# Optimization experiments

Hardware: AMD Instinct MI355X
Metric: run time of the kernel (lower is better)

The kernel has to match this reference:

```python
import jax, jax.numpy as jnp
from jax import lax
import numpy as np

D_MODEL = 1024
N_HEADS = 16
D_STATE = D_MODEL // N_HEADS  # 64
EPS = 1e-6


def setup_inputs() -> dict:
    key = jax.random.key(0)
    ks = jax.random.split(key, 8)
    B, S = 4, 4096
    s = 1.0 / np.sqrt(D_MODEL)
    return {
        "x": jax.random.normal(ks[0], (B, S, D_MODEL), dtype=jnp.float32),
        "state": jnp.zeros((B, N_HEADS, D_STATE), dtype=jnp.float32),
        "norm_w": jnp.ones((D_MODEL,), dtype=jnp.float32),
        "Wp": jax.random.normal(ks[1], (D_MODEL, 3 * N_HEADS * D_STATE), dtype=jnp.float32) * s,
        "bp": jax.random.normal(ks[2], (3 * N_HEADS * D_STATE,), dtype=jnp.float32) * 0.01,
        "Wg": jax.random.normal(ks[3], (D_MODEL, D_MODEL), dtype=jnp.float32) * s,
        "bg": jax.random.normal(ks[4], (D_MODEL,), dtype=jnp.float32) * 0.01,
        "Wo": jax.random.normal(ks[5], (D_MODEL, D_MODEL), dtype=jnp.float32) * s,
        "bo": jax.random.normal(ks[6], (D_MODEL,), dtype=jnp.float32) * 0.01,
    }


def reference(x, state, norm_w, Wp, bp, Wg, bg, Wo, bo):
    B, S, D = x.shape
    # RMSNorm
    rms = jnp.sqrt(jnp.mean(x * x, axis=-1, keepdims=True) + EPS)
    xn = norm_w * x / rms
    # input-dependent gate and SSM parameters (all per-timestep, vectorized)
    gate = jax.nn.sigmoid(xn @ Wg + bg)                        # (B,S,D)
    p = (xn @ Wp + bp).reshape(B, S, N_HEADS, 3, D_STATE)
    delta = jax.nn.sigmoid(p[..., 0, :])                       # (B,S,H,Ds)
    Bt = p[..., 1, :]
    Ct = p[..., 2, :]
    # sequential recurrence h_{t+1} = delta_t * h_t + B_t via lax.scan over time
    def step(h, db):
        d, b = db
        h = d * h + b
        return h, h
    dT = jnp.moveaxis(delta, 1, 0)  # (S,B,H,Ds)
    bT = jnp.moveaxis(Bt, 1, 0)
    new_state, hs = lax.scan(step, state, (dT, bT))
    hs = jnp.moveaxis(hs, 0, 1)     # (B,S,H,Ds)
    ssm = (Ct * hs).reshape(B, S, D)
    mixed = gate * ssm + (1.0 - gate) * xn
    y = mixed @ Wo + bo + x         # out_proj + residual (dropout=0)
    return y, new_state
```

## Files before the change

### kernel.cpp

```cpp
#include <hip/hip_runtime.h>
#include <hip/hip_bf16.h>
#include <cstdint>
#include <cstddef>

#define D_MODEL 1024
#define N_HEADS 16
#define D_STATE 64
#define SEQ 4096
#define BATCH 4
#define M_TOK (BATCH * SEQ)
#define N1 4096
#define CLEN 128
#define NCH (SEQ / CLEN)
#define NCHAN (BATCH * D_MODEL)

typedef __attribute__((ext_vector_type(8))) short bf16x8;
typedef __attribute__((ext_vector_type(4))) float f32x4;

__device__ __forceinline__ float sigmoidf_(float x) {
    return 1.0f / (1.0f + __expf(-x));
}

__device__ __forceinline__ void async_load16(const void* g, void* l) {
    __builtin_amdgcn_global_load_lds(
        (__attribute__((address_space(1))) void*)(g),
        (__attribute__((address_space(3))) void*)(l), 16, 0, 0);
}

__global__ __launch_bounds__(256) void transpose_cvt(
    const float* __restrict__ src, __hip_bfloat16* __restrict__ dst,
    int K, int N)
{
    __shared__ float tile[32][33];
    int n0 = blockIdx.x * 32, k0 = blockIdx.y * 32;
    int tx = threadIdx.x, ty = threadIdx.y;
#pragma unroll
    for (int j = 0; j < 32; j += 8)
        tile[ty + j][tx] = src[(size_t)(k0 + ty + j) * N + n0 + tx];
    __syncthreads();
#pragma unroll
    for (int j = 0; j < 32; j += 8)
        dst[(size_t)(n0 + ty + j) * K + k0 + tx] = __float2bfloat16(tile[tx][ty + j]);
}

__global__ __launch_bounds__(256) void rmsnorm_kernel(
    const float* __restrict__ x, const float* __restrict__ w,
    __hip_bfloat16* __restrict__ xn)
{
    int m = blockIdx.x;
    int tid = threadIdx.x;
    const float4* xr = (const float4*)(x + (size_t)m * D_MODEL);
    float4 v = xr[tid];
    float ss = v.x * v.x + v.y * v.y + v.z * v.z + v.w * v.w;
#pragma unroll
    for (int o = 32; o >= 1; o >>= 1) ss += __shfl_xor(ss, o, 64);
    __shared__ float red[4];
    int wave = tid >> 6, lane = tid & 63;
    if (lane == 0) red[wave] = ss;
    __syncthreads();
    float tot = red[0] + red[1] + red[2] + red[3];
    float scale = rsqrtf(tot * (1.0f / D_MODEL) + 1e-6f);
    const float4* wr = (const float4*)w;
    float4 wv = wr[tid];
    __hip_bfloat16 o4[4];
    o4[0] = __float2bfloat16(wv.x * v.x * scale);
    o4[1] = __float2bfloat16(wv.y * v.y * scale);
    o4[2] = __float2bfloat16(wv.z * v.z * scale);
    o4[3] = __float2bfloat16(wv.w * v.w * scale);
    *(uint64_t*)(xn + (size_t)m * D_MODEL + tid * 4) = *(uint64_t*)o4;
}


template <int MODE>
__global__ __launch_bounds__(512, 2) void gemm256(
    const __hip_bfloat16* __restrict__ A,
    const __hip_bfloat16* __restrict__ Bt,
    const float* __restrict__ bias0,
    const float* __restrict__ bias1,
    void* __restrict__ outp, int N, int K)
{
    extern __shared__ short lds[];
    const int tid = threadIdx.x;
    const int wave = tid >> 6, lane = tid & 63;
    const int fr = lane & 15, fq = lane >> 4;
    const int frx = fr & 7;
    const int wm = (wave >> 2) * 128;
    const int wn = (wave & 3) * 64;

    const int gx = gridDim.x;
    const int nwg = gx * gridDim.y;
    const int orig = blockIdx.y * gx + blockIdx.x;
    const int swz = (orig & 7) * (nwg >> 3) + (orig >> 3);
    const int m0 = (swz / gx) * 256;
    const int n0 = (swz % gx) * 256;

    const int rb = tid >> 3, p8 = tid & 7;
    const int lsl = p8 ^ (rb & 7);
    const short* Ag0 = (const short*)A + (size_t)(m0 + rb) * K + lsl * 8;
    const short* Bg0 = (const short*)Bt + (size_t)(n0 + rb) * K + lsl * 8;
    const int stL = rb * 64 + p8 * 8;

    const int NT = K >> 6;

    f32x4 acc[2][4][4];
#pragma unroll
    for (int h = 0; h < 2; ++h)
#pragma unroll
        for (int i = 0; i < 4; ++i)
#pragma unroll
            for (int j = 0; j < 4; ++j)
                acc[h][i][j] = (f32x4){0.f, 0.f, 0.f, 0.f};

    {
        short* la = lds;
        short* lb = lds + 16384;
        async_load16(Bg0 + (size_t)(0 * 64) * K, lb + stL + 0 * 4096);
        async_load16(Bg0 + (size_t)(1 * 64) * K, lb + stL + 1 * 4096);
        async_load16(Bg0 + (size_t)(2 * 64) * K, lb + stL + 2 * 4096);
        async_load16(Bg0 + (size_t)(3 * 64) * K, lb + stL + 3 * 4096);
        async_load16(Ag0 + (size_t)(0 * 64) * K, la + stL + 0 * 4096);
        async_load16(Ag0 + (size_t)(2 * 64) * K, la + stL + 2 * 4096);
        async_load16(Ag0 + (size_t)(1 * 64) * K, la + stL + 1 * 4096);
        async_load16(Ag0 + (size_t)(3 * 64) * K, la + stL + 3 * 4096);
    }
    asm volatile("s_waitcnt vmcnt(2)" ::: "memory");
    __builtin_amdgcn_s_barrier();
    __builtin_amdgcn_sched_barrier(0);

#define LDA(h, i, kk) (*(const bf16x8*)&Ab[(wm + (h)*64 + (i)*16 + fr) * 64 + \
                                           (((kk)*4 + fq) ^ frx) * 8])
#define LDB(j, kk)    (*(const bf16x8*)&Bb[(wn + (j)*16 + fr) * 64 + \
                                           (((kk)*4 + fq) ^ frx) * 8])
#define STAGE_A(c) async_load16(AgN + (size_t)((c) * 64) * K, laN + stL + (c) * 4096)
#define STAGE_B(c) async_load16(BgN + (size_t)((c) * 64) * K, lbN + stL + (c) * 4096)

    for (int t = 0; t < NT; ++t) {
        const short* Ab = lds + ((t & 1) ? 32768 : 0);
        const short* Bb = Ab + 16384;
        short* laN = lds + ((t & 1) ? 0 : 32768);
        short* lbN = laN + 16384;
        const short* AgN = Ag0 + (size_t)(t + 1) * 64;
        const short* BgN = Bg0 + (size_t)(t + 1) * 64;
        const bool pf = (t + 1 < NT);

        bf16x8 af[4][2], b0[2][2], b1[2][2];

#pragma unroll
        for (int i = 0; i < 4; ++i) { af[i][0] = LDA(0, i, 0); af[i][1] = LDA(0, i, 1); }
#pragma unroll
        for (int j = 0; j < 2; ++j) { b0[j][0] = LDB(j, 0); b0[j][1] = LDB(j, 1); }
        if (pf) { STAGE_B(0); STAGE_B(1); }
        __builtin_amdgcn_s_barrier();
        __builtin_amdgcn_sched_barrier(0);
        __builtin_amdgcn_s_setprio(1);
#pragma unroll
        for (int i = 0; i < 4; ++i)
#pragma unroll
            for (int j = 0; j < 2; ++j) {
                acc[0][i][j] = __builtin_amdgcn_mfma_f32_16x16x32_bf16(af[i][0], b0[j][0], acc[0][i][j], 0, 0, 0);
                acc[0][i][j] = __builtin_amdgcn_mfma_f32_16x16x32_bf16(af[i][1], b0[j][1], acc[0][i][j], 0, 0, 0);
            }
        __builtin_amdgcn_s_setprio(0);
        __builtin_amdgcn_sched_barrier(0);
        __builtin_amdgcn_s_barrier();
        __builtin_amdgcn_sched_barrier(0);

#pragma unroll
        for (int j = 0; j < 2; ++j) { b1[j][0] = LDB(2 + j, 0); b1[j][1] = LDB(2 + j, 1); }
        if (pf) { STAGE_B(2); STAGE_B(3); }
        __builtin_amdgcn_s_barrier();
        __builtin_amdgcn_sched_barrier(0);
        __builtin_amdgcn_s_setprio(1);
#pragma unroll
        for (int i = 0; i < 4; ++i)
#pragma unroll
            for (int j = 0; j < 2; ++j) {
                acc[0][i][2 + j] = __builtin_amdgcn_mfma_f32_16x16x32_bf16(af[i][0], b1[j][0], acc[0][i][2 + j], 0, 0, 0);
                acc[0][i][2 + j] = __builtin_amdgcn_mfma_f32_16x16x32_bf16(af[i][1], b1[j][1], acc[0][i][2 + j], 0, 0, 0);
            }
        __builtin_amdgcn_s_setprio(0);
        __builtin_amdgcn_sched_barrier(0);
        if (pf) { asm volatile("s_waitcnt vmcnt(4)" ::: "memory"); }
        else    { asm volatile("s_waitcnt vmcnt(0)" ::: "memory"); }
        __builtin_amdgcn_s_barrier();
        __builtin_amdgcn_sched_barrier(0);

#pragma unroll
        for (int i = 0; i < 4; ++i) { af[i][0] = LDA(1, i, 0); af[i][1] = LDA(1, i, 1); }
        if (pf) { STAGE_A(0); STAGE_A(2); }
        __builtin_amdgcn_s_barrier();
        __builtin_amdgcn_sched_barrier(0);
        __builtin_amdgcn_s_setprio(1);
#pragma unroll
        for (int i = 0; i < 4; ++i)
#pragma unroll
            for (int j = 0; j < 2; ++j) {
                acc[1][i][j] = __builtin_amdgcn_mfma_f32_16x16x32_bf16(af[i][0], b0[j][0], acc[1][i][j], 0, 0, 0);
                acc[1][i][j] = __builtin_amdgcn_mfma_f32_16x16x32_bf16(af[i][1], b0[j][1], acc[1][i][j], 0, 0, 0);
            }
        __builtin_amdgcn_s_setprio(0);
        __builtin_amdgcn_sched_barrier(0);
        __builtin_amdgcn_s_barrier();
        __builtin_amdgcn_sched_barrier(0);

        if (pf) {
            STAGE_A(1); STAGE_A(3);
            asm volatile("s_waitcnt vmcnt(2)" ::: "memory");
        }
        __builtin_amdgcn_s_barrier();
        __builtin_amdgcn_sched_barrier(0);
        __builtin_amdgcn_s_setprio(1);
#pragma unroll
        for (int i = 0; i < 4; ++i)
#pragma unroll
            for (int j = 0; j < 2; ++j) {
                acc[1][i][2 + j] = __builtin_amdgcn_mfma_f32_16x16x32_bf16(af[i][0], b1[j][0], acc[1][i][2 + j], 0, 0, 0);
                acc[1][i][2 + j] = __builtin_amdgcn_mfma_f32_16x16x32_bf16(af[i][1], b1[j][1], acc[1][i][2 + j], 0, 0, 0);
            }
        __builtin_amdgcn_s_setprio(0);
        __builtin_amdgcn_sched_barrier(0);
        __builtin_amdgcn_s_barrier();
        __builtin_amdgcn_sched_barrier(0);
    }
#undef LDA
#undef LDB
#undef STAGE_A
#undef STAGE_B

    if constexpr (MODE == 0) {
        __hip_bfloat16* O = (__hip_bfloat16*)outp;
        float bv[4];
#pragma unroll
        for (int j = 0; j < 4; ++j) {
            int gcol = n0 + wn + j * 16 + fr;
            bv[j] = (gcol < D_MODEL) ? bias0[gcol] : bias1[gcol - D_MODEL];
        }
#pragma unroll
        for (int h = 0; h < 2; ++h)
#pragma unroll
            for (int i = 0; i < 4; ++i)
#pragma unroll
                for (int r = 0; r < 4; ++r) {
                    int grow = m0 + wm + h * 64 + i * 16 + fq * 4 + r;
                    __hip_bfloat16* orow = O + (size_t)grow * N + n0 + wn + fr;
#pragma unroll
                    for (int j = 0; j < 4; ++j)
                        orow[j * 16] = __float2bfloat16(acc[h][i][j][r] + bv[j]);
                }
    } else {
        float* O = (float*)outp;
#pragma unroll
        for (int h = 0; h < 2; ++h)
#pragma unroll
            for (int i = 0; i < 4; ++i)
#pragma unroll
                for (int r = 0; r < 4; ++r) {
                    int grow = m0 + wm + h * 64 + i * 16 + fq * 4 + r;
#pragma unroll
                    for (int j = 0; j < 4; ++j) {
                        int gcol = n0 + wn + j * 16 + fr;
                        O[(size_t)grow * N + gcol] =
                            acc[h][i][j][r] + bias0[gcol] + bias1[(size_t)grow * D_MODEL + gcol];
                    }
                }
    }
}

__global__ __launch_bounds__(256) void scan_part1(
    const __hip_bfloat16* __restrict__ out1,
    float* __restrict__ Abuf, float* __restrict__ Bbuf)
{
    int g = blockIdx.x * 256 + threadIdx.x;
    int chan = g & (NCHAN - 1);
    int c = g >> 12;
    int b = chan >> 10;
    int hd = chan & 1023;
    int h = hd >> 6, d = hd & 63;
    size_t tok0 = (size_t)b * SEQ + (size_t)c * CLEN;
    const __hip_bfloat16* pd = out1 + tok0 * N1 + D_MODEL + h * 192 + d;
    float a = 1.0f, hloc = 0.0f;
#pragma unroll 4
    for (int s = 0; s < CLEN; s++) {
        float dp = __bfloat162float(pd[0]);
        float bt = __bfloat162float(pd[64]);
        float sd = sigmoidf_(dp);
        a *= sd;
        hloc = sd * hloc + bt;
        pd += N1;
    }
    Abuf[c * NCHAN + chan] = a;
    Bbuf[c * NCHAN + chan] = hloc;
}

__global__ __launch_bounds__(256) void scan_comb(
    const float* __restrict__ Abuf, const float* __restrict__ Bbuf,
    const float* __restrict__ state, float* __restrict__ Pbuf,
    float* __restrict__ new_state)
{
    int chan = blockIdx.x * 256 + threadIdx.x;
    float hp = state[chan];
#pragma unroll
    for (int c = 0; c < NCH; c++) {
        Pbuf[c * NCHAN + chan] = hp;
        hp = Abuf[c * NCHAN + chan] * hp + Bbuf[c * NCHAN + chan];
    }
    new_state[chan] = hp;
}

__global__ __launch_bounds__(256) void scan_apply(
    const __hip_bfloat16* __restrict__ out1,
    const __hip_bfloat16* __restrict__ xn,
    const float* __restrict__ Pbuf,
    __hip_bfloat16* __restrict__ mixed)
{
    int g = blockIdx.x * 256 + threadIdx.x;
    int chan = g & (NCHAN - 1);
    int c = g >> 12;
    int b = chan >> 10;
    int hd = chan & 1023;
    int h = hd >> 6, d = hd & 63;
    size_t tok0 = (size_t)b * SEQ + (size_t)c * CLEN;
    const __hip_bfloat16* rbase = out1 + tok0 * N1;
    const __hip_bfloat16* xbase = xn + tok0 * D_MODEL + hd;
    __hip_bfloat16* mbase = mixed + tok0 * D_MODEL + hd;
    const int pcol = D_MODEL + h * 192 + d;
    float hh = Pbuf[c * NCHAN + chan];
#pragma unroll 4
    for (int s = 0; s < CLEN; s++) {
        const __hip_bfloat16* r = rbase + (size_t)s * N1;
        float dp = __bfloat162float(r[pcol]);
        float bt = __bfloat162float(r[pcol + 64]);
        float ct = __bfloat162float(r[pcol + 128]);
        float gp = __bfloat162float(r[hd]);
        float sd = sigmoidf_(dp);
        hh = sd * hh + bt;
        float gg = sigmoidf_(gp);
        float xv = __bfloat162float(xbase[(size_t)s * D_MODEL]);
        mbase[(size_t)s * D_MODEL] = __float2bfloat16(gg * (ct * hh) + (1.0f - gg) * xv);
    }
}

extern "C" void kernel_launch(void* const* d_in, const int* in_sizes, int n_in,
                              void* d_out, int out_size, void* d_ws, size_t ws_size,
                              hipStream_t stream) {
    const float* x      = (const float*)d_in[0];
    const float* state  = (const float*)d_in[1];
    const float* norm_w = (const float*)d_in[2];
    const float* Wp     = (const float*)d_in[3];
    const float* bp     = (const float*)d_in[4];
    const float* Wg     = (const float*)d_in[5];
    const float* bg     = (const float*)d_in[6];
    const float* Wo     = (const float*)d_in[7];
    const float* bo     = (const float*)d_in[8];
    float* out = (float*)d_out;

    __hip_bfloat16* W1T   = (__hip_bfloat16*)d_ws;
    __hip_bfloat16* WoT   = W1T + (size_t)N1 * D_MODEL;
    __hip_bfloat16* xnb   = WoT + (size_t)D_MODEL * D_MODEL;
    __hip_bfloat16* out1  = xnb + (size_t)M_TOK * D_MODEL;
    __hip_bfloat16* mixed = out1 + (size_t)M_TOK * N1;
    float* Abuf = (float*)(mixed + (size_t)M_TOK * D_MODEL);
    float* Bbuf = Abuf + (size_t)NCHAN * NCH;
    float* Pbuf = Bbuf + (size_t)NCHAN * NCH;

    static bool attr_set = false;
    if (!attr_set) {
        hipFuncSetAttribute(reinterpret_cast<const void*>(&gemm256<0>),
                            hipFuncAttributeMaxDynamicSharedMemorySize, 131072);
        hipFuncSetAttribute(reinterpret_cast<const void*>(&gemm256<1>),
                            hipFuncAttributeMaxDynamicSharedMemorySize, 131072);
        attr_set = true;
    }

    dim3 tb(32, 8);
    transpose_cvt<<<dim3(1024 / 32, 1024 / 32), tb, 0, stream>>>(Wg, W1T, 1024, 1024);
    transpose_cvt<<<dim3(3072 / 32, 1024 / 32), tb, 0, stream>>>(
        Wp, W1T + (size_t)D_MODEL * D_MODEL, 1024, 3072);
    transpose_cvt<<<dim3(1024 / 32, 1024 / 32), tb, 0, stream>>>(Wo, WoT, 1024, 1024);

    rmsnorm_kernel<<<M_TOK, 256, 0, stream>>>(x, norm_w, xnb);

    gemm256<0><<<dim3(N1 / 256, M_TOK / 256), 512, 131072, stream>>>(
        xnb, W1T, bg, bp, (void*)out1, N1, D_MODEL);

    scan_part1<<<(NCHAN * NCH) / 256, 256, 0, stream>>>(out1, Abuf, Bbuf);
    scan_comb<<<NCHAN / 256, 256, 0, stream>>>(
        Abuf, Bbuf, state, Pbuf, out + (size_t)M_TOK * D_MODEL);
    scan_apply<<<(NCHAN * NCH) / 256, 256, 0, stream>>>(out1, xnb, Pbuf, mixed);

    gemm256<1><<<dim3(D_MODEL / 256, M_TOK / 256), 512, 131072, stream>>>(
        mixed, WoT, bo, x, (void*)out, D_MODEL, D_MODEL);
}
```

Baseline: 394.1 us.

## Software-pipeline LDS fragment reads across iterations and cut per-iteration barriers

Restructures the GEMM main loop so that the A/B register fragments for the next k-tile are preloaded at the end of the current iteration. LDS reads are interleaved between MFMA blocks instead of sitting in their own barrier-separated phases. Most of the workgroup barriers per iteration are removed, leaving one after the B wait and one after the final A wait. This aims to hide LDS latency and sync overhead, at the cost of more live fragment registers (afA/afB). It also risks a race on reuse of the staged buffers, since fewer barriers protect them.

Result: no change. 391.4 us (-0.7%).

```diff
diff --git a/kernel.cpp b/kernel.cpp
--- a/kernel.cpp
+++ b/kernel.cpp
@@ -127,12 +127,23 @@
     __builtin_amdgcn_s_barrier();
     __builtin_amdgcn_sched_barrier(0);
 
-#define LDA(h, i, kk) (*(const bf16x8*)&Ab[(wm + (h)*64 + (i)*16 + fr) * 64 + \
-                                           (((kk)*4 + fq) ^ frx) * 8])
-#define LDB(j, kk)    (*(const bf16x8*)&Bb[(wn + (j)*16 + fr) * 64 + \
-                                           (((kk)*4 + fq) ^ frx) * 8])
+#define LDA_(base, h, i, kk) (*(const bf16x8*)&(base)[(wm + (h)*64 + (i)*16 + fr) * 64 + \
+                                                      (((kk)*4 + fq) ^ frx) * 8])
+#define LDB_(base, j, kk)    (*(const bf16x8*)&(base)[(wn + (j)*16 + fr) * 64 + \
+                                                      (((kk)*4 + fq) ^ frx) * 8])
 #define STAGE_A(c) async_load16(AgN + (size_t)((c) * 64) * K, laN + stL + (c) * 4096)
 #define STAGE_B(c) async_load16(BgN + (size_t)((c) * 64) * K, lbN + stL + (c) * 4096)
+
+    bf16x8 afA[4][2], afB[4][2], b0[2][2], b1[2][2];
+
+    {
+        const short* Ab = lds;
+        const short* Bb = lds + 16384;
+#pragma unroll
+        for (int i = 0; i < 4; ++i) { afA[i][0] = LDA_(Ab, 0, i, 0); afA[i][1] = LDA_(Ab, 0, i, 1); }
+#pragma unroll
+        for (int j = 0; j < 2; ++j) { b0[j][0] = LDB_(Bb, j, 0); b0[j][1] = LDB_(Bb, j, 1); }
+    }
 
     for (int t = 0; t < NT; ++t) {
         const short* Ab = lds + ((t & 1) ? 32768 : 0);
@@ -143,87 +154,75 @@
         const short* BgN = Bg0 + (size_t)(t + 1) * 64;
         const bool pf = (t + 1 < NT);
 
-        bf16x8 af[4][2], b0[2][2], b1[2][2];
-
-#pragma unroll
-        for (int i = 0; i < 4; ++i) { af[i][0] = LDA(0, i, 0); af[i][1] = LDA(0, i, 1); }
-#pragma unroll
-        for (int j = 0; j < 2; ++j) { b0[j][0] = LDB(j, 0); b0[j][1] = LDB(j, 1); }
         if (pf) { STAGE_B(0); STAGE_B(1); }
-        __builtin_amdgcn_s_barrier();
-        __builtin_amdgcn_sched_barrier(0);
+#pragma unroll
+        for (int j = 0; j < 2; ++j) { b1[j][0] = LDB_(Bb, 2 + j, 0); b1[j][1] = LDB_(Bb, 2 + j, 1); }
         __builtin_amdgcn_s_setprio(1);
 #pragma unroll
         for (int i = 0; i < 4; ++i)
 #pragma unroll
             for (int j = 0; j < 2; ++j) {
-                acc[0][i][j] = __builtin_amdgcn_mfma_f32_16x16x32_bf16(af[i][0], b0[j][0], acc[0][i][j], 0, 0, 0);
-                acc[0][i][j] = __builtin_amdgcn_mfma_f32_16x16x32_bf16(af[i][1], b0[j][1], acc[0][i][j], 0, 0, 0);
+                acc[0][i][j] = __builtin_amdgcn_mfma_f32_16x16x32_bf16(afA[i][0], b0[j][0], acc[0][i][j], 0, 0, 0);
+                acc[0][i][j] = __builtin_amdgcn_mfma_f32_16x16x32_bf16(afA[i][1], b0[j][1], acc[0][i][j], 0, 0, 0);
             }
         __builtin_amdgcn_s_setprio(0);
         __builtin_amdgcn_sched_barrier(0);
-        __builtin_amdgcn_s_barrier();
-        __builtin_amdgcn_sched_barrier(0);
-
-#pragma unroll
-        for (int j = 0; j < 2; ++j) { b1[j][0] = LDB(2 + j, 0); b1[j][1] = LDB(2 + j, 1); }
+
         if (pf) { STAGE_B(2); STAGE_B(3); }
-        __builtin_amdgcn_s_barrier();
-        __builtin_amdgcn_sched_barrier(0);
-        __builtin_amdgcn_s_setprio(1);
-#pragma unroll
-        for (int i = 0; i < 4; ++i)
-#pragma unroll
-            for (int j = 0; j < 2; ++j) {
-                acc[0][i][2 + j] = __builtin_amdgcn_mfma_f32_16x16x32_bf16(af[i][0], b1[j][0], acc[0][i][2 + j], 0, 0, 0);
-                acc[0][i][2 + j] = __builtin_amdgcn_mfma_f32_16x16x32_bf16(af[i][1], b1[j][1], acc[0][i][2 + j], 0, 0, 0);
-            }
-        __builtin_amdgcn_s_setprio(0);
-        __builtin_amdgcn_sched_barrier(0);
         if (pf) { asm volatile("s_waitcnt vmcnt(4)" ::: "memory"); }
         else    { asm volatile("s_waitcnt vmcnt(0)" ::: "memory"); }
         __builtin_amdgcn_s_barrier();
         __builtin_amdgcn_sched_barrier(0);
-
-#pragma unroll
-        for (int i = 0; i < 4; ++i) { af[i][0] = LDA(1, i, 0); af[i][1] = LDA(1, i, 1); }
-        if (pf) { STAGE_A(0); STAGE_A(2); }
-        __builtin_amdgcn_s_barrier();
-        __builtin_amdgcn_sched_barrier(0);
+#pragma unroll
+        for (int i = 0; i < 4; ++i) { afB[i][0] = LDA_(Ab, 1, i, 0); afB[i][1] = LDA_(Ab, 1, i, 1); }
         __builtin_amdgcn_s_setprio(1);
 #pragma unroll
         for (int i = 0; i < 4; ++i)
 #pragma unroll
             for (int j = 0; j < 2; ++j) {
-                acc[1][i][j] = __builtin_amdgcn_mfma_f32_16x16x32_bf16(af[i][0], b0[j][0], acc[1][i][j], 0, 0, 0);
-                acc[1][i][j] = __builtin_amdgcn_mfma_f32_16x16x32_bf16(af[i][1], b0[j][1], acc[1][i][j], 0, 0, 0);
+                acc[0][i][2 + j] = __builtin_amdgcn_mfma_f32_16x16x32_bf16(afA[i][0], b1[j][0], acc[0][i][2 + j], 0, 0, 0);
+                acc[0][i][2 + j] = __builtin_amdgcn_mfma_f32_16x16x32_bf16(afA[i][1], b1[j][1], acc[0][i][2 + j], 0, 0, 0);
             }
         __builtin_amdgcn_s_setprio(0);
         __builtin_amdgcn_sched_barrier(0);
-        __builtin_amdgcn_s_barrier();
+
+        if (pf) { STAGE_A(0); STAGE_A(2); }
+        __builtin_amdgcn_s_setprio(1);
+#pragma unroll
+        for (int i = 0; i < 4; ++i)
+#pragma unroll
+            for (int j = 0; j < 2; ++j) {
+                acc[1][i][j] = __builtin_amdgcn_mfma_f32_16x16x32_bf16(afB[i][0], b0[j][0], acc[1][i][j], 0, 0, 0);
+                acc[1][i][j] = __builtin_amdgcn_mfma_f32_16x16x32_bf16(afB[i][1], b0[j][1], acc[1][i][j], 0, 0, 0);
+            }
+        __builtin_amdgcn_s_setprio(0);
         __builtin_amdgcn_sched_barrier(0);
 
         if (pf) {
             STAGE_A(1); STAGE_A(3);
             asm volatile("s_waitcnt vmcnt(2)" ::: "memory");
+            __builtin_amdgcn_s_barrier();
+            __builtin_amdgcn_sched_barrier(0);
+            const short* AbN = laN;
+            const short* BbN = lbN;
+#pragma unroll
+            for (int i = 0; i < 4; ++i) { afA[i][0] = LDA_(AbN, 0, i, 0); afA[i][1] = LDA_(AbN, 0, i, 1); }
+#pragma unroll
+            for (int j = 0; j < 2; ++j) { b0[j][0] = LDB_(BbN, j, 0); b0[j][1] = LDB_(BbN, j, 1); }
         }
-        __builtin_amdgcn_s_barrier();
-        __builtin_amdgcn_sched_barrier(0);
         __builtin_amdgcn_s_setprio(1);
 #pragma unroll
         for (int i = 0; i < 4; ++i)
 #pragma unroll
             for (int j = 0; j < 2; ++j) {
-                acc[1][i][2 + j] = __builtin_amdgcn_mfma_f32_16x16x32_bf16(af[i][0], b1[j][0], acc[1][i][2 + j], 0, 0, 0);
-                acc[1][i][2 + j] = __builtin_amdgcn_mfma_f32_16x16x32_bf16(af[i][1], b1[j][1], acc[1][i][2 + j], 0, 0, 0);
+                acc[1][i][2 + j] = __builtin_amdgcn_mfma_f32_16x16x32_bf16(afB[i][0], b1[j][0], acc[1][i][2 + j], 0, 0, 0);
+                acc[1][i][2 + j] = __builtin_amdgcn_mfma_f32_16x16x32_bf16(afB[i][1], b1[j][1], acc[1][i][2 + j], 0, 0, 0);
             }
         __builtin_amdgcn_s_setprio(0);
         __builtin_amdgcn_sched_barrier(0);
-        __builtin_amdgcn_s_barrier();
-        __builtin_amdgcn_sched_barrier(0);
-    }
-#undef LDA
-#undef LDB
+    }
+#undef LDA_
+#undef LDB_
 #undef STAGE_A
 #undef STAGE_B
 
```
